# Performance work log

Measured on AMD Instinct MI355X. Metric: run time of the kernel, lower is better.

The kernel has to match this reference:

```python
import jax, jax.numpy as jnp
import numpy as np

N_NODES = 20000
DIM = 128
N_EDGES = 500000
BATCH = 16384
EPS = 1e-6  # torch.nn.PairwiseDistance default eps


def setup_inputs() -> dict:
    key = jax.random.key(0)
    k = jax.random.split(key, 8)
    edges = jax.random.randint(k[0], (2, N_EDGES), 0, N_NODES, dtype=jnp.int64 if jax.config.jax_enable_x64 else jnp.int32)
    nodes_p_star = jnp.sort(jax.random.randint(k[1], (BATCH,), 0, N_NODES))
    nodes_p = jnp.sort(jax.random.randint(k[2], (BATCH,), 0, N_NODES))
    # learned parameters, init in [-1, 1) as in the torch module
    beta_p = 2.0 * jax.random.uniform(k[3], (N_NODES,), dtype=jnp.float32) - 1.0
    beta_p_star = 2.0 * jax.random.uniform(k[4], (N_NODES,), dtype=jnp.float32) - 1.0
    p = 2.0 * jax.random.uniform(k[5], (N_NODES, DIM), dtype=jnp.float32) - 1.0
    p_star = 2.0 * jax.random.uniform(k[6], (N_NODES, DIM), dtype=jnp.float32) - 1.0
    return {
        "edges": edges,
        "nodes_p_star": nodes_p_star,
        "nodes_p": nodes_p,
        "beta_p": beta_p,
        "beta_p_star": beta_p_star,
        "p": p,
        "p_star": p_star,
    }


def reference(edges, nodes_p_star, nodes_p, beta_p, beta_p_star, p, p_star):
    # ---- link term: sum over observed edges of (beta - dist) ----
    beta_pair = beta_p_star[edges[0]] + beta_p[edges[1]]  # [E]
    diff = p[edges[0]] - p_star[edges[1]]                 # [E, D]
    # torch PairwiseDistance adds eps to the difference before the norm
    z_dist = jnp.sqrt(jnp.sum((diff + EPS) ** 2, axis=-1))
    link_term = jnp.sum(beta_pair - z_dist)

    # ---- non-link term: triu-masked sum of exp(beta - cdist) ----
    bps = beta_p_star[nodes_p_star]   # [Ns]
    bp = beta_p[nodes_p]              # [Np]
    ps = p_star[nodes_p_star]         # [Ns, D]
    pp = p[nodes_p]                   # [Np, D]
    beta_mat = bps[None, :] + bp[:, None]          # [Np, Ns]
    # cdist(ps, pp) -> [Ns, Np] via Gram trick
    sq = (jnp.sum(ps * ps, axis=-1)[:, None]
          + jnp.sum(pp * pp, axis=-1)[None, :]
          - 2.0 * jnp.einsum('nd,md->nm', ps, pp))
    dist_mat = jnp.sqrt(jnp.maximum(sq, 0.0))      # [Ns, Np]
    intensity = jnp.exp(beta_mat.T - dist_mat)     # [Ns, Np]
    non_link = jnp.sum(jnp.triu(intensity, k=1))

    return -(link_term - non_link)
```

## Files before the change

kernel.cpp:

```cpp
#include <hip/hip_runtime.h>
#include <hip/hip_bf16.h>
#include <hip/hip_fp8.h>

#define N_NODES 20000
#define DIM 128
#define N_EDGES 500000
#define BATCH 16384
#define EPS 1e-6f
#define L2E 1.4426950408889634f

typedef float f32x4 __attribute__((ext_vector_type(4)));
typedef float f32x2 __attribute__((ext_vector_type(2)));
typedef long long i64_t;

__device__ __forceinline__ float fast_sqrtf(float x) {
#if __has_builtin(__builtin_amdgcn_sqrtf)
    return __builtin_amdgcn_sqrtf(x);
#else
    return sqrtf(x);
#endif
}
__device__ __forceinline__ float fast_exp2f(float x) {
#if __has_builtin(__builtin_amdgcn_exp2f)
    return __builtin_amdgcn_exp2f(x);
#else
    return exp2f(x);
#endif
}

__device__ __forceinline__ unsigned pack4_fp8(float a, float b, float c, float d) {
#if __has_builtin(__builtin_amdgcn_cvt_pk_fp8_f32)
    unsigned v = 0;
    v = __builtin_amdgcn_cvt_pk_fp8_f32(a, b, v, false);
    v = __builtin_amdgcn_cvt_pk_fp8_f32(c, d, v, true);
    return v;
#else
    __hip_fp8_e4m3 x0(a), x1(b), x2(c), x3(d);
    return (unsigned)x0.__x | ((unsigned)x1.__x << 8) |
           ((unsigned)x2.__x << 16) | ((unsigned)x3.__x << 24);
#endif
}

template <bool HI>
__device__ __forceinline__ f32x2 unpack2_fp8(unsigned v) {
#if __has_builtin(__builtin_amdgcn_cvt_pk_f32_fp8)
    return __builtin_amdgcn_cvt_pk_f32_fp8((int)v, HI);
#else
    __hip_fp8_e4m3 t0, t1;
    t0.__x = (unsigned char)(HI ? (v >> 16) : v);
    t1.__x = (unsigned char)(HI ? (v >> 24) : (v >> 8));
    f32x2 r; r.x = (float)t0; r.y = (float)t1;
    return r;
#endif
}

#define OFF_A8   0
#define OFF_B8   2097152
#define OFF_N2S  4194304
#define OFF_N2P  4259840
#define OFF_BPS  4325376
#define OFF_BP   4390912
#define OFF_P8   4456448
#define OFF_PS8  7016448
#define OFF_END  9576448

__global__ __launch_bounds__(256) void prep_kernel(
    const float* __restrict__ p, const float* __restrict__ p_star,
    const float* __restrict__ beta_p, const float* __restrict__ beta_ps,
    const int* __restrict__ nodes_ps, const int* __restrict__ nodes_p,
    unsigned char* __restrict__ A8, float* __restrict__ n2A, float* __restrict__ bA2,
    unsigned char* __restrict__ B8, float* __restrict__ n2B, float* __restrict__ bB2,
    unsigned char* __restrict__ p8, unsigned char* __restrict__ ps8,
    float* __restrict__ out)
{
    const int bx = blockIdx.x;
    if (bx == 0 && threadIdx.x == 0) out[0] = 0.f;
    if (bx < 4096) {
        const int g = threadIdx.x & 31;
        const int r8 = threadIdx.x >> 5;
        const bool isA = bx < 2048;
        int row = (isA ? bx : bx - 2048) * 8 + r8;
        int id = isA ? nodes_ps[row] : nodes_p[row];
        const float* src = isA ? p_star : p;
        float4 v = ((const float4*)(src + (size_t)id * DIM))[g];
        unsigned pk = pack4_fp8(v.x, v.y, v.z, v.w);
        unsigned char* dst = isA ? A8 : B8;
        ((unsigned*)(dst + (size_t)row * DIM))[g] = pk;
        float nrm = v.x * v.x + v.y * v.y + v.z * v.z + v.w * v.w;
        #pragma unroll
        for (int m = 16; m >= 1; m >>= 1) nrm += __shfl_xor(nrm, m, 32);
        if (g == 0) {
            if (isA) { n2A[row] = nrm; bA2[row] = L2E * beta_ps[id]; }
            else     { n2B[row] = nrm; bB2[row] = L2E * beta_p[id]; }
        }
    } else {
        int b = bx - 4096;
        const bool isP = b < 1250;
        const float* src = isP ? p : p_star;
        unsigned char* dst = isP ? p8 : ps8;
        int base = (isP ? b : b - 1250) * 512 + threadIdx.x;
        #pragma unroll
        for (int u = 0; u < 2; ++u) {
            int f4 = base + u * 256;
            float4 v = ((const float4*)src)[f4];
            ((unsigned*)dst)[f4] = pack4_fp8(v.x, v.y, v.z, v.w);
        }
    }
}

#define LSTRIDE 144
__global__ __launch_bounds__(512, 4) void main_kernel(
    const unsigned char* __restrict__ Ag, const unsigned char* __restrict__ Bg,
    const float* __restrict__ n2A, const float* __restrict__ n2B,
    const float* __restrict__ bA2, const float* __restrict__ bB2,
    const int* __restrict__ edges,
    const float* __restrict__ beta_p, const float* __restrict__ beta_ps,
    const unsigned char* __restrict__ p8, const unsigned char* __restrict__ ps8,
    float* __restrict__ out)
{
    const int bx = blockIdx.x, by = blockIdx.y;
    int ti, tj;
    const int len = 128 - by;
    if (bx < len) { ti = by; tj = by + bx; }
    else          { ti = 127 - by; tj = 127 - (bx - len); }
    const int i0 = ti * 128, j0 = tj * 128;
    const int bid = by * 129 + bx;
    const bool diag = (ti == tj);

    __shared__ __align__(16) unsigned char As[128 * LSTRIDE];
    __shared__ __align__(16) unsigned char Bs[128 * LSTRIDE];
    __shared__ float smr[8];

    const int tid = threadIdx.x;
    const int lane = tid & 63;
    const int w = tid >> 6;
    const int wm = w & 3;
    const int wn = w >> 2;
    const int quad = lane >> 4;
    const int lr = lane & 15;

    float lsum = 0.f;
    const int le = bid * 64 + w * 8 + (lane >> 3);
    const int lch = lane & 7;
    const bool ev = (le < N_EDGES);
    uint4 ua, ub;
    float ebeta = 0.f;
    if (ev) {
        int e0 = edges[le];
        int e1 = edges[N_EDGES + le];
        ua = *(const uint4*)(p8 + (size_t)e0 * DIM + lch * 16);
        ub = *(const uint4*)(ps8 + (size_t)e1 * DIM + lch * 16);
        if (lch == 0) ebeta = beta_ps[e0] + beta_p[e1];
    }

    const int ilo = i0 + wm * 32, jlo = j0 + wn * 64;
    float4 n2i[2], bi[2];
    #pragma unroll
    for (int mi = 0; mi < 2; ++mi) {
        n2i[mi] = *(const float4*)&n2A[ilo + mi * 16 + quad * 4];
        bi[mi]  = *(const float4*)&bA2[ilo + mi * 16 + quad * 4];
    }
    float n2j[4], bj[4];
    #pragma unroll
    for (int ni = 0; ni < 4; ++ni) {
        n2j[ni] = n2B[jlo + ni * 16 + lr];
        bj[ni]  = bB2[jlo + ni * 16 + lr];
    }

    #pragma unroll
    for (int c = tid; c < 1024; c += 512) {
        int row = c >> 3, col = (c & 7) * 16;
        *(uint4*)&As[row * LSTRIDE + col] = *(const uint4*)(Ag + (size_t)(i0 + row) * DIM + col);
        *(uint4*)&Bs[row * LSTRIDE + col] = *(const uint4*)(Bg + (size_t)(j0 + row) * DIM + col);
    }
    __syncthreads();

    int cls = 0;
    if (diag) cls = (wn == 0) ? (wm >= 2 ? 2 : 1) : (wm >= 2 ? 1 : 0);

    if (cls != 2) {
        f32x4 acc[2][4] = {};
        #pragma unroll
        for (int ks = 0; ks < 4; ++ks) {
            int koff = ks * 32 + quad * 8;
            i64_t af[2], bf[4];
            #pragma unroll
            for (int u = 0; u < 2; ++u)
                af[u] = *(const i64_t*)&As[(wm * 32 + u * 16 + lr) * LSTRIDE + koff];
            #pragma unroll
            for (int v = 0; v < 4; ++v)
                bf[v] = *(const i64_t*)&Bs[(wn * 64 + v * 16 + lr) * LSTRIDE + koff];
            #pragma unroll
            for (int mi = 0; mi < 2; ++mi)
                #pragma unroll
                for (int ni = 0; ni < 4; ++ni)
                    acc[mi][ni] = __builtin_amdgcn_mfma_f32_16x16x32_fp8_fp8(af[mi], bf[ni], acc[mi][ni], 0, 0, 0);
        }

        if (cls == 0) {
            #pragma unroll
            for (int mi = 0; mi < 2; ++mi)
                #pragma unroll
                for (int ni = 0; ni < 4; ++ni) {
                    f32x4 d = acc[mi][ni];
                    #pragma unroll
                    for (int r = 0; r < 4; ++r) {
                        float tt = ((const float*)&n2i[mi])[r] + n2j[ni];
                        float sq = fmaxf(fmaf(d[r], -2.f, tt), 0.f);
                        float arg = fmaf(fast_sqrtf(sq), -L2E, ((const float*)&bi[mi])[r] + bj[ni]);
                        lsum += fast_exp2f(arg);
                    }
                }
        } else {
            #pragma unroll
            for (int mi = 0; mi < 2; ++mi)
                #pragma unroll
                for (int ni = 0; ni < 4; ++ni) {
                    f32x4 d = acc[mi][ni];
                    #pragma unroll
                    for (int r = 0; r < 4; ++r) {
                        int ig = ilo + mi * 16 + quad * 4 + r;
                        int jg = jlo + ni * 16 + lr;
                        float tt = ((const float*)&n2i[mi])[r] + n2j[ni];
                        float sq = fmaxf(fmaf(d[r], -2.f, tt), 0.f);
                        float arg = fmaf(fast_sqrtf(sq), -L2E, ((const float*)&bi[mi])[r] + bj[ni]);
                        float ex = fast_exp2f(arg);
                        if (jg > ig) lsum += ex;
                    }
                }
        }
    }

    if (ev) {
        float s = 0.f;
        #pragma unroll
        for (int d = 0; d < 4; ++d) {
            unsigned va = ((const unsigned*)&ua)[d];
            unsigned vb = ((const unsigned*)&ub)[d];
            f32x2 a0 = unpack2_fp8<false>(va), a1 = unpack2_fp8<true>(va);
            f32x2 b0 = unpack2_fp8<false>(vb), b1 = unpack2_fp8<true>(vb);
            float t0 = a0.x - b0.x + EPS, t1 = a0.y - b0.y + EPS;
            float t2 = a1.x - b1.x + EPS, t3 = a1.y - b1.y + EPS;
            s = fmaf(t0, t0, s); s = fmaf(t1, t1, s);
            s = fmaf(t2, t2, s); s = fmaf(t3, t3, s);
        }
        #pragma unroll
        for (int m = 4; m >= 1; m >>= 1) s += __shfl_xor(s, m, 8);
        if (lch == 0) lsum -= ebeta - fast_sqrtf(s);
    }

    #pragma unroll
    for (int m = 32; m >= 1; m >>= 1) lsum += __shfl_xor(lsum, m, 64);
    if (lane == 0) smr[w] = lsum;
    __syncthreads();
    if (tid == 0) {
        float t = 0.f;
        #pragma unroll
        for (int i = 0; i < 8; ++i) t += smr[i];
        atomicAdd(out, t);
    }
}

extern "C" void kernel_launch(void* const* d_in, const int* in_sizes, int n_in,
                              void* d_out, int out_size, void* d_ws, size_t ws_size,
                              hipStream_t stream) {
    const int* edges = (const int*)d_in[0];
    const int* nodes_p_star = (const int*)d_in[1];
    const int* nodes_p = (const int*)d_in[2];
    const float* beta_p = (const float*)d_in[3];
    const float* beta_p_star = (const float*)d_in[4];
    const float* p = (const float*)d_in[5];
    const float* p_star = (const float*)d_in[6];

    char* ws = (char*)d_ws;
    unsigned char* A8 = (unsigned char*)(ws + OFF_A8);
    unsigned char* B8 = (unsigned char*)(ws + OFF_B8);
    float* n2s = (float*)(ws + OFF_N2S);
    float* n2p = (float*)(ws + OFF_N2P);
    float* bps2 = (float*)(ws + OFF_BPS);
    float* bp2 = (float*)(ws + OFF_BP);
    unsigned char* p8 = (unsigned char*)(ws + OFF_P8);
    unsigned char* ps8 = (unsigned char*)(ws + OFF_PS8);

    prep_kernel<<<6596, 256, 0, stream>>>(
        p, p_star, beta_p, beta_p_star, nodes_p_star, nodes_p,
        A8, n2s, bps2, B8, n2p, bp2, p8, ps8, (float*)d_out);

    main_kernel<<<dim3(129, 64), 512, 0, stream>>>(
        A8, B8, n2s, n2p, bps2, bp2,
        edges, beta_p, beta_p_star, p8, ps8, (float*)d_out);
}
```

Measured before the change: 197.3 us.

## Split prep into full-table fp8 pass plus gather, reorder loads, pack epilogue math

```diff
diff --git a/kernel.cpp b/kernel.cpp
--- a/kernel.cpp
+++ b/kernel.cpp
@@ -27,6 +27,14 @@
     return exp2f(x);
 #endif
 }
+__device__ __forceinline__ f32x2 splat2(float s) { f32x2 r = {s, s}; return r; }
+__device__ __forceinline__ f32x2 max2(f32x2 a, f32x2 b) {
+#if __has_builtin(__builtin_elementwise_max)
+    return __builtin_elementwise_max(a, b);
+#else
+    f32x2 r; r.x = fmaxf(a.x, b.x); r.y = fmaxf(a.y, b.y); return r;
+#endif
+}
 
 __device__ __forceinline__ unsigned pack4_fp8(float a, float b, float c, float d) {
 #if __has_builtin(__builtin_amdgcn_cvt_pk_fp8_f32)
@@ -54,57 +62,70 @@
 #endif
 }
 
-#define OFF_A8   0
-#define OFF_B8   2097152
-#define OFF_N2S  4194304
-#define OFF_N2P  4259840
-#define OFF_BPS  4325376
-#define OFF_BP   4390912
-#define OFF_P8   4456448
-#define OFF_PS8  7016448
-#define OFF_END  9576448
-
-__global__ __launch_bounds__(256) void prep_kernel(
-    const float* __restrict__ p, const float* __restrict__ p_star,
+#define OFF_N2A   0
+#define OFF_N2B   65536
+#define OFF_BA    131072
+#define OFF_BB    196608
+#define OFF_A8    262144
+#define OFF_B8    2359296
+#define OFF_P8    4456448
+#define OFF_PS8   7016448
+#define OFF_N2PT  9576448
+#define OFF_N2PST 9656448
+#define OFF_BTP   9736448
+#define OFF_BTPS  9816448
+#define OFF_END   9896448
+
+__global__ __launch_bounds__(256) void prep1_kernel(
+    const float* __restrict__ p, const float* __restrict__ ps,
     const float* __restrict__ beta_p, const float* __restrict__ beta_ps,
-    const int* __restrict__ nodes_ps, const int* __restrict__ nodes_p,
-    unsigned char* __restrict__ A8, float* __restrict__ n2A, float* __restrict__ bA2,
-    unsigned char* __restrict__ B8, float* __restrict__ n2B, float* __restrict__ bB2,
     unsigned char* __restrict__ p8, unsigned char* __restrict__ ps8,
+    float* __restrict__ n2pt, float* __restrict__ n2pst,
+    float* __restrict__ btp, float* __restrict__ btps,
     float* __restrict__ out)
 {
-    const int bx = blockIdx.x;
-    if (bx == 0 && threadIdx.x == 0) out[0] = 0.f;
-    if (bx < 4096) {
+    const int b = blockIdx.x;
+    if (b == 0 && threadIdx.x == 0) out[0] = 0.f;
+    if (b < 5000) {
+        const bool isP = b < 2500;
+        const float* src = isP ? p : ps;
+        unsigned char* dst = isP ? p8 : ps8;
+        float* n2t = isP ? n2pt : n2pst;
         const int g = threadIdx.x & 31;
-        const int r8 = threadIdx.x >> 5;
-        const bool isA = bx < 2048;
-        int row = (isA ? bx : bx - 2048) * 8 + r8;
-        int id = isA ? nodes_ps[row] : nodes_p[row];
-        const float* src = isA ? p_star : p;
-        float4 v = ((const float4*)(src + (size_t)id * DIM))[g];
-        unsigned pk = pack4_fp8(v.x, v.y, v.z, v.w);
-        unsigned char* dst = isA ? A8 : B8;
-        ((unsigned*)(dst + (size_t)row * DIM))[g] = pk;
+        const int row = (isP ? b : b - 2500) * 8 + (threadIdx.x >> 5);
+        float4 v = ((const float4*)(src + (size_t)row * DIM))[g];
+        ((unsigned*)(dst + (size_t)row * DIM))[g] = pack4_fp8(v.x, v.y, v.z, v.w);
         float nrm = v.x * v.x + v.y * v.y + v.z * v.z + v.w * v.w;
         #pragma unroll
         for (int m = 16; m >= 1; m >>= 1) nrm += __shfl_xor(nrm, m, 32);
-        if (g == 0) {
-            if (isA) { n2A[row] = nrm; bA2[row] = L2E * beta_ps[id]; }
-            else     { n2B[row] = nrm; bB2[row] = L2E * beta_p[id]; }
-        }
+        if (g == 0) n2t[row] = nrm;
     } else {
-        int b = bx - 4096;
-        const bool isP = b < 1250;
-        const float* src = isP ? p : p_star;
-        unsigned char* dst = isP ? p8 : ps8;
-        int base = (isP ? b : b - 1250) * 512 + threadIdx.x;
-        #pragma unroll
-        for (int u = 0; u < 2; ++u) {
-            int f4 = base + u * 256;
-            float4 v = ((const float4*)src)[f4];
-            ((unsigned*)dst)[f4] = pack4_fp8(v.x, v.y, v.z, v.w);
-        }
+        int t = (b - 5000) * 256 + threadIdx.x;
+        if (t < N_NODES) btp[t] = L2E * beta_p[t];
+        else if (t < 2 * N_NODES) btps[t - N_NODES] = L2E * beta_ps[t - N_NODES];
+    }
+}
+
+__global__ __launch_bounds__(256) void prep2_kernel(
+    const int* __restrict__ nodes_ps, const int* __restrict__ nodes_p,
+    const unsigned char* __restrict__ p8, const unsigned char* __restrict__ ps8,
+    const float* __restrict__ n2pt, const float* __restrict__ n2pst,
+    const float* __restrict__ btp, const float* __restrict__ btps,
+    unsigned char* __restrict__ A8, float* __restrict__ n2A, float* __restrict__ bA2,
+    unsigned char* __restrict__ B8, float* __restrict__ n2B, float* __restrict__ bB2)
+{
+    const int b = blockIdx.x;
+    const bool isA = b < 512;
+    const int row = (isA ? b : b - 512) * 32 + (threadIdx.x >> 3);
+    const int l8 = threadIdx.x & 7;
+    const int id = isA ? nodes_ps[row] : nodes_p[row];
+    const unsigned char* tbl = isA ? ps8 : p8;
+    unsigned char* dst = isA ? A8 : B8;
+    uint4 v = *(const uint4*)(tbl + (size_t)id * DIM + l8 * 16);
+    *(uint4*)(dst + (size_t)row * DIM + l8 * 16) = v;
+    if (l8 == 0) {
+        if (isA) { n2A[row] = n2pst[id]; bA2[row] = btps[id]; }
+        else     { n2B[row] = n2pt[id];  bB2[row] = btp[id]; }
     }
 }
 
@@ -139,20 +160,30 @@
     const int quad = lane >> 4;
     const int lr = lane & 15;
 
-    float lsum = 0.f;
     const int le = bid * 64 + w * 8 + (lane >> 3);
     const int lch = lane & 7;
     const bool ev = (le < N_EDGES);
-    uint4 ua, ub;
+    int e0 = 0, e1 = 0;
     float ebeta = 0.f;
     if (ev) {
-        int e0 = edges[le];
-        int e1 = edges[N_EDGES + le];
+        e0 = edges[le];
+        e1 = edges[N_EDGES + le];
+        if (lch == 0) ebeta = beta_ps[e0] + beta_p[e1];
+    }
+
+    #pragma unroll
+    for (int c = tid; c < 1024; c += 512) {
+        int row = c >> 3, col = (c & 7) * 16;
+        *(uint4*)&As[row * LSTRIDE + col] = *(const uint4*)(Ag + (size_t)(i0 + row) * DIM + col);
+        *(uint4*)&Bs[row * LSTRIDE + col] = *(const uint4*)(Bg + (size_t)(j0 + row) * DIM + col);
+    }
+    __syncthreads();
+
+    uint4 ua = {0,0,0,0}, ub = {0,0,0,0};
+    if (ev) {
         ua = *(const uint4*)(p8 + (size_t)e0 * DIM + lch * 16);
         ub = *(const uint4*)(ps8 + (size_t)e1 * DIM + lch * 16);
-        if (lch == 0) ebeta = beta_ps[e0] + beta_p[e1];
-    }
-
+    }
     const int ilo = i0 + wm * 32, jlo = j0 + wn * 64;
     float4 n2i[2], bi[2];
     #pragma unroll
@@ -167,17 +198,11 @@
         bj[ni]  = bB2[jlo + ni * 16 + lr];
     }
 
-    #pragma unroll
-    for (int c = tid; c < 1024; c += 512) {
-        int row = c >> 3, col = (c & 7) * 16;
-        *(uint4*)&As[row * LSTRIDE + col] = *(const uint4*)(Ag + (size_t)(i0 + row) * DIM + col);
-        *(uint4*)&Bs[row * LSTRIDE + col] = *(const uint4*)(Bg + (size_t)(j0 + row) * DIM + col);
-    }
-    __syncthreads();
-
     int cls = 0;
     if (diag) cls = (wn == 0) ? (wm >= 2 ? 2 : 1) : (wm >= 2 ? 1 : 0);
 
+    float lsum = 0.f;
+    f32x2 lsum2 = {0.f, 0.f};
     if (cls != 2) {
         f32x4 acc[2][4] = {};
         #pragma unroll
@@ -199,18 +224,26 @@
 
         if (cls == 0) {
             #pragma unroll
-            for (int mi = 0; mi < 2; ++mi)
+            for (int mi = 0; mi < 2; ++mi) {
+                f32x2 n2iA = {n2i[mi].x, n2i[mi].y}, n2iB = {n2i[mi].z, n2i[mi].w};
+                f32x2 biA  = {bi[mi].x,  bi[mi].y},  biB  = {bi[mi].z,  bi[mi].w};
                 #pragma unroll
                 for (int ni = 0; ni < 4; ++ni) {
                     f32x4 d = acc[mi][ni];
-                    #pragma unroll
-                    for (int r = 0; r < 4; ++r) {
-                        float tt = ((const float*)&n2i[mi])[r] + n2j[ni];
-                        float sq = fmaxf(fmaf(d[r], -2.f, tt), 0.f);
-                        float arg = fmaf(fast_sqrtf(sq), -L2E, ((const float*)&bi[mi])[r] + bj[ni]);
-                        lsum += fast_exp2f(arg);
-                    }
+                    f32x2 d0 = {d[0], d[1]}, d1 = {d[2], d[3]};
+                    f32x2 bsum0 = biA + splat2(bj[ni]);
+                    f32x2 bsum1 = biB + splat2(bj[ni]);
+                    f32x2 sq0 = max2(d0 * splat2(-2.f) + (n2iA + splat2(n2j[ni])), splat2(0.f));
+                    f32x2 sq1 = max2(d1 * splat2(-2.f) + (n2iB + splat2(n2j[ni])), splat2(0.f));
+                    f32x2 dist0 = {fast_sqrtf(sq0.x), fast_sqrtf(sq0.y)};
+                    f32x2 dist1 = {fast_sqrtf(sq1.x), fast_sqrtf(sq1.y)};
+                    f32x2 arg0 = dist0 * splat2(-L2E) + bsum0;
+                    f32x2 arg1 = dist1 * splat2(-L2E) + bsum1;
+                    f32x2 ex0 = {fast_exp2f(arg0.x), fast_exp2f(arg0.y)};
+                    f32x2 ex1 = {fast_exp2f(arg1.x), fast_exp2f(arg1.y)};
+                    lsum2 += ex0 + ex1;
                 }
+            }
         } else {
             #pragma unroll
             for (int mi = 0; mi < 2; ++mi)
@@ -230,6 +263,7 @@
                 }
         }
     }
+    lsum += lsum2.x + lsum2.y;
 
     if (ev) {
         float s = 0.f;
@@ -273,20 +307,27 @@
     const float* p_star = (const float*)d_in[6];
 
     char* ws = (char*)d_ws;
+    float* n2A = (float*)(ws + OFF_N2A);
+    float* n2B = (float*)(ws + OFF_N2B);
+    float* bA2 = (float*)(ws + OFF_BA);
+    float* bB2 = (float*)(ws + OFF_BB);
     unsigned char* A8 = (unsigned char*)(ws + OFF_A8);
     unsigned char* B8 = (unsigned char*)(ws + OFF_B8);
-    float* n2s = (float*)(ws + OFF_N2S);
-    float* n2p = (float*)(ws + OFF_N2P);
-    float* bps2 = (float*)(ws + OFF_BPS);
-    float* bp2 = (float*)(ws + OFF_BP);
     unsigned char* p8 = (unsigned char*)(ws + OFF_P8);
     unsigned char* ps8 = (unsigned char*)(ws + OFF_PS8);
-
-    prep_kernel<<<6596, 256, 0, stream>>>(
-        p, p_star, beta_p, beta_p_star, nodes_p_star, nodes_p,
-        A8, n2s, bps2, B8, n2p, bp2, p8, ps8, (float*)d_out);
+    float* n2pt = (float*)(ws + OFF_N2PT);
+    float* n2pst = (float*)(ws + OFF_N2PST);
+    float* btp = (float*)(ws + OFF_BTP);
+    float* btps = (float*)(ws + OFF_BTPS);
+
+    prep1_kernel<<<5157, 256, 0, stream>>>(
+        p, p_star, beta_p, beta_p_star, p8, ps8, n2pt, n2pst, btp, btps, (float*)d_out);
+
+    prep2_kernel<<<1024, 256, 0, stream>>>(
+        nodes_p_star, nodes_p, p8, ps8, n2pt, n2pst, btp, btps,
+        A8, n2A, bA2, B8, n2B, bB2);
 
     main_kernel<<<dim3(129, 64), 512, 0, stream>>>(
-        A8, B8, n2s, n2p, bps2, bp2,
+        A8, B8, n2A, n2B, bA2, bB2,
         edges, beta_p, beta_p_star, p8, ps8, (float*)d_out);
 }
```

Result: no change. 198.7 us (+0.7%).
